# Performance work log

Hardware: AMD Instinct MI355X
Metric: run time of the kernel (lower is better)

The kernel has to match this reference:

```python
import jax, jax.numpy as jnp
import numpy as np

EPS = 1e-12
WA = 0.002


def _radial_bins(h: int, w: int):
    """Static (numpy) replication of torch _radial_masks: centered integer radial
    bins, then fftshift'd (matching the original code exactly)."""
    y = np.linspace(-(h // 2), h // 2 - (1 if h % 2 == 0 else 0), h)
    x = np.linspace(-(w // 2), w // 2 - (1 if w % 2 == 0 else 0), w)
    yy, xx = np.meshgrid(y, x, indexing='ij')
    dist = np.sqrt(xx ** 2 + yy ** 2)
    max_bin = int(dist.max())  # torch: int(max) then clamp -> no-op since dist>=0
    bins = np.clip(dist.astype(np.int32), 0, max_bin)
    bins = np.fft.fftshift(bins)
    return jnp.asarray(bins.reshape(-1)), max_bin


def setup_inputs() -> dict:
    key = jax.random.key(0)
    B, H, W = 16, 1024, 1024
    prob_cg = jax.random.uniform(key, (B, 1, H, W), dtype=jnp.float32)
    return {"prob_cg": prob_cg}


def reference(prob_cg) -> jnp.ndarray:
    B, C, H, W = prob_cg.shape
    seg, max_bin = _radial_bins(H, W)  # [H*W] int32 bin ids, static max_bin
    n_bins = max_bin + 1

    # Power spectrum P(f) = |fftshift(fft2(p))|^2 / N.
    # (torch code fftshifts all dims incl. batch; that is a pure batch permutation
    #  and the final loss is a mean over batch, so shifting only spatial axes is
    #  mathematically identical.)
    p = prob_cg[:, 0].astype(jnp.float32)
    fv = jnp.fft.fftshift(jnp.fft.fft2(p, axes=(-2, -1)), axes=(-2, -1))
    power = (fv.real ** 2 + fv.imag ** 2) / (H * W)  # [B,H,W]

    # Radial segment-mean over integer-radius annuli (replaces the O(B*R*H*W)
    # double loop with a single O(B*H*W) scatter-add).
    flat = power.reshape(B, H * W)
    sums = jax.vmap(lambda v: jax.ops.segment_sum(v, seg, num_segments=n_bins))(flat)
    counts = jax.ops.segment_sum(jnp.ones((H * W,), jnp.float32), seg, num_segments=n_bins)
    radial = jnp.where(counts > 0, sums / jnp.maximum(counts, 1.0), 0.0)  # [B,n_bins]

    # Broadcast radial mean back to the grid and accumulate squared deviation.
    radial_expanded = radial[:, seg].reshape(B, H, W)
    loss = jnp.mean(jnp.sum((power - radial_expanded + EPS) ** 2, axis=(-2, -1)))
    return WA * loss
```

## Files before the change

kernel.cpp:

```cpp
#include <hip/hip_runtime.h>
#include <math.h>

#define NB 16
#define NPAIR 8
#define NBINS 725
#define NPIX (1024*1024)

#define SLOT(idx, c) ((idx)*9 + (c) + ((idx)>>5))
#define SH_SIZE 9248
#define C45 0.70710678118654752f

__device__ __forceinline__ unsigned bf16rn(float f) {
    unsigned u = __float_as_uint(f);
    return (u + 0x7FFFu + ((u >> 16) & 1u)) >> 16;
}
__device__ __forceinline__ unsigned pk2(float2 v) {
    return bf16rn(v.x) | (bf16rn(v.y) << 16);
}
__device__ __forceinline__ float2 up2(unsigned v) {
    return make_float2(__uint_as_float(v << 16), __uint_as_float(v & 0xFFFF0000u));
}

__device__ __forceinline__ constexpr int rev5(int j) {
    return ((j&1)<<4) | ((j&2)<<2) | (j&4) | ((j&8)>>2) | ((j&16)>>4);
}

__device__ __forceinline__ void fft32(float2* r) {
    const float wr[16] = {1.f, 0.98078528f, 0.92387953f, 0.83146961f,
                          0.70710678f, 0.55557023f, 0.38268343f, 0.19509032f,
                          0.f, -0.19509032f, -0.38268343f, -0.55557023f,
                          -0.70710678f, -0.83146961f, -0.92387953f, -0.98078528f};
    const float wi[16] = {0.f, -0.19509032f, -0.38268343f, -0.55557023f,
                          -0.70710678f, -0.83146961f, -0.92387953f, -0.98078528f,
                          -1.f, -0.98078528f, -0.92387953f, -0.83146961f,
                          -0.70710678f, -0.55557023f, -0.38268343f, -0.19509032f};
    #pragma unroll
    for (int s = 1; s <= 5; ++s) {
        const int half = 1 << (s - 1);
        #pragma unroll
        for (int g = 0; g < 32; g += (1 << s)) {
            #pragma unroll
            for (int j = 0; j < half; ++j) {
                const int a = j << (5 - s);
                int i1 = g + j, i2 = i1 + half;
                float2 u = r[i1], v = r[i2], vw;
                if (a == 0)       vw = v;
                else if (a == 8)  vw = make_float2(v.y, -v.x);
                else if (a == 4)  vw = make_float2(C45 * (v.x + v.y), C45 * (v.y - v.x));
                else if (a == 12) vw = make_float2(C45 * (v.y - v.x), -C45 * (v.x + v.y));
                else {
                    const float cw = wr[a], sw = wi[a];
                    vw = make_float2(v.x * cw - v.y * sw, v.x * sw + v.y * cw);
                }
                r[i1] = make_float2(u.x + vw.x, u.y + vw.y);
                r[i2] = make_float2(u.x - vw.x, u.y - vw.y);
            }
        }
    }
}

__device__ __forceinline__ void twiddle1024(float2* r, int n1) {
    float sn, cs;
    sincosf((float)n1 * -0.006135923151542565f, &sn, &cs);
    float wx = 1.f, wy = 0.f;
    #pragma unroll
    for (int k2 = 0; k2 < 32; ++k2) {
        float2 s = r[k2];
        r[k2] = make_float2(s.x * wx - s.y * wy, s.x * wy + s.y * wx);
        float nx = wx * cs - wy * sn;
        wy = wx * sn + wy * cs;
        wx = nx;
    }
}

__device__ __forceinline__ int ibin(int d2) {
    int bin = (int)sqrtf((float)d2);
    if ((bin + 1) * (bin + 1) <= d2) ++bin;
    else if (bin * bin > d2) --bin;
    return bin;
}

__device__ __forceinline__ int col_of(int k, int c) {
    if (k == 0) return (c < 4) ? c : ((c == 4) ? 512 : 1028 - c);
    int a = k << 2;
    return (c < 4) ? (a + c) : (1017 + c - a);
}
__device__ __forceinline__ int mir_of(int k, int c) {
    if (k == 0) return (c == 0 || c == 4) ? c : ((c < 4) ? c + 4 : c - 4);
    return 7 - c;
}

__global__ __launch_bounds__(256, 4) void fft_rows(const float* __restrict__ in,
                                                   unsigned* __restrict__ spec,
                                                   float* __restrict__ cntp) {
    __shared__ unsigned sh[SH_SIZE];
    __shared__ float hc[NBINS];
    int tid = threadIdx.x, blk = blockIdx.x;
    int p = blk >> 7, y0 = (blk & 127) << 3;
    if (p == 0)
        for (int i = tid; i < NBINS; i += 256) hc[i] = 0.f;
    int n1 = tid & 31, c = tid >> 5;
    const float* xr = in + (((size_t)(2 * p)) << 20) + ((size_t)(y0 + c) << 10);
    const float* yr = xr + (1u << 20);
    float2 r[32];
    #pragma unroll
    for (int j = 0; j < 32; ++j) {
        int n = n1 + (rev5(j) << 5);
        r[j] = make_float2(xr[n], yr[n]);
    }
    fft32(r);
    twiddle1024(r, n1);
    int sb = 9 * n1 + c;
    #pragma unroll
    for (int k2 = 0; k2 < 32; ++k2) sh[sb + 289 * k2] = pk2(r[k2]);
    __syncthreads();
    int k2 = tid & 31;
    int rb = 289 * k2 + c;
    #pragma unroll
    for (int j = 0; j < 32; ++j) r[j] = up2(sh[rb + 9 * rev5(j)]);
    fft32(r);
    __syncthreads();
    int wb = 9 * k2 + c;
    #pragma unroll
    for (int k1 = 0; k1 < 32; ++k1) sh[wb + 289 * k1] = pk2(r[k1]);
    __syncthreads();
    unsigned* base = spec + (((size_t)p) << 20);
    for (int rep = 0; rep < 32; ++rep) {
        int idx = (rep << 8) + tid;
        int kcol = idx >> 3, cc = idx & 7;
        base[((size_t)kcol << 10) + y0 + cc] = sh[SLOT(kcol, cc)];
    }
    if (p == 0) {
        int g = blk;
        int row = (g << 2) + (tid >> 6);
        int xb = (tid & 63) << 4;
        int dy = row - 512, dy2 = dy * dy;
        int curbin = -1;
        float a = 0.f;
        #pragma unroll 4
        for (int j = 0; j < 16; ++j) {
            int x = xb + j;
            float w = 2.f;
            if (row == 0) w = (x > 512 || x == 0) ? 0.f : ((x == 512) ? 1.f : 2.f);
            int dx = x - 512;
            int bin = ibin(dy2 + dx * dx);
            if (bin == curbin) a += w;
            else {
                if (curbin >= 0 && a != 0.f) atomicAdd(&hc[curbin], a);
                curbin = bin; a = w;
            }
        }
        if (curbin >= 0 && a != 0.f) atomicAdd(&hc[curbin], a);
        if (g == 0) {
            int xb2 = tid << 2;
            int curb = -1;
            float aa = 0.f;
            #pragma unroll
            for (int j = 0; j < 4; ++j) {
                int xx = xb2 + j;
                if (xx > 512) continue;
                float w = ((xx & 511) == 0) ? 1.f : 2.f;
                int bin = 512 - xx;
                if (bin == curb) aa += w;
                else {
                    if (curb >= 0 && aa != 0.f) atomicAdd(&hc[curb], aa);
                    curb = bin; aa = w;
                }
            }
            if (curb >= 0 && aa != 0.f) atomicAdd(&hc[curb], aa);
        }
        __syncthreads();
        for (int i = tid; i < NBINS; i += 256)
            cntp[(size_t)g * NBINS + i] = hc[i];
    }
}

__global__ __launch_bounds__(256, 3) void fft_cols_hist(const unsigned* __restrict__ spec,
                                                        float* __restrict__ s2buf,
                                                        float* __restrict__ partial) {
    __shared__ unsigned sh[SH_SIZE];
    __shared__ float hs0[NBINS], hs1[NBINS];
    __shared__ float wred[8];
    int tid = threadIdx.x, blk = blockIdx.x;
    int p = blk >> 7, k = blk & 127;
    for (int i = tid; i < NBINS; i += 256) { hs0[i] = 0.f; hs1[i] = 0.f; }
    int n1 = tid & 31, c = tid >> 5;
    const unsigned* base = spec + (((size_t)p) << 20);
    const unsigned* colp = base + ((size_t)col_of(k, c) << 10);
    float2 r[32];
    #pragma unroll
    for (int j = 0; j < 32; ++j) r[j] = up2(colp[n1 + (rev5(j) << 5)]);
    fft32(r);
    twiddle1024(r, n1);
    int sb = 9 * n1 + c;
    #pragma unroll
    for (int q = 0; q < 32; ++q) sh[sb + 289 * q] = pk2(r[q]);
    __syncthreads();
    int k2 = tid & 31;
    int rb = 289 * k2 + c;
    #pragma unroll
    for (int j = 0; j < 32; ++j) r[j] = up2(sh[rb + 9 * rev5(j)]);
    __syncthreads();
    fft32(r);
    int wb = 9 * k2 + c;
    #pragma unroll
    for (int k1 = 0; k1 < 32; ++k1) sh[wb + 289 * k1] = pk2(r[k1]);
    __syncthreads();
    const float inv = 1.0f / (float)NPIX;
    int cl = tid >> 5, chunk = tid & 31;
    int xcol = col_of(k, cl), mc = mir_of(k, cl);
    int dxv = xcol - 512, dx2 = dxv * dxv;
    bool xs = ((xcol & 511) == 0), xhi = (xcol > 512);
    float s2e = 0.f, s2o = 0.f;
    int curbin = -1;
    float a0 = 0.f, a1 = 0.f;
    int ky0 = chunk << 4;
    #pragma unroll 4
    for (int j = 0; j < 16; ++j) {
        int ky = ky0 + j;
        float w = 2.f;
        if (ky == 0) w = xhi ? 0.f : ((xcol == 0) ? 0.f : (xs ? 1.f : 2.f));
        int my = (1024 - ky) & 1023;
        float2 f1 = up2(sh[SLOT(ky, cl)]);
        float2 f2 = up2(sh[SLOT(my, mc)]);
        float xr = 0.5f * (f1.x + f2.x), xi = 0.5f * (f1.y - f2.y);
        float yr = 0.5f * (f1.y + f2.y), yi = 0.5f * (f2.x - f1.x);
        float pe = (xr * xr + xi * xi) * inv;
        float po = (yr * yr + yi * yi) * inv;
        int dy = ky - 512;
        int bin = ibin(dy * dy + dx2);
        float v0 = w * pe, v1 = w * po;
        s2e += v0 * pe;
        s2o += v1 * po;
        if (bin == curbin) { a0 += v0; a1 += v1; }
        else {
            if (curbin >= 0) { atomicAdd(&hs0[curbin], a0); atomicAdd(&hs1[curbin], a1); }
            curbin = bin; a0 = v0; a1 = v1;
        }
    }
    if (curbin >= 0) { atomicAdd(&hs0[curbin], a0); atomicAdd(&hs1[curbin], a1); }
    if ((tid & 31) == 0) {
        int cl2 = tid >> 5;
        int x2 = col_of(k, cl2);
        if (x2 <= 512) {
            int mc2 = mir_of(k, cl2);
            float w = ((x2 & 511) == 0) ? 1.f : 2.f;
            float2 f1 = up2(sh[SLOT(512, cl2)]);
            float2 f2 = up2(sh[SLOT(512, mc2)]);
            float xr = 0.5f * (f1.x + f2.x), xi = 0.5f * (f1.y - f2.y);
            float yr = 0.5f * (f1.y + f2.y), yi = 0.5f * (f2.x - f1.x);
            float pe = (xr * xr + xi * xi) * inv;
            float po = (yr * yr + yi * yi) * inv;
            float v0 = w * pe, v1 = w * po;
            s2e += v0 * pe;
            s2o += v1 * po;
            int bin = (x2 < 512) ? 512 - x2 : 0;
            atomicAdd(&hs0[bin], v0);
            atomicAdd(&hs1[bin], v1);
        }
    }
    #pragma unroll
    for (int off = 32; off > 0; off >>= 1) {
        s2e += __shfl_down(s2e, off);
        s2o += __shfl_down(s2o, off);
    }
    if ((tid & 63) == 0) { wred[tid >> 6] = s2e; wred[4 + (tid >> 6)] = s2o; }
    __syncthreads();
    if (tid == 0) s2buf[2 * blk]     = wred[0] + wred[1] + wred[2] + wred[3];
    if (tid == 1) s2buf[2 * blk + 1] = wred[4] + wred[5] + wred[6] + wred[7];
    float* pe = partial + ((size_t)(2 * p) * 128 + k) * NBINS;
    float* po = partial + ((size_t)(2 * p + 1) * 128 + k) * NBINS;
    for (int i = tid; i < NBINS; i += 256) {
        pe[i] = hs0[i];
        po[i] = hs1[i];
    }
}

__global__ __launch_bounds__(256) void reduce_loss(const float* __restrict__ partial,
                                                   const float* __restrict__ cntp,
                                                   float* __restrict__ rowval) {
    int b = blockIdx.x / 3, band = blockIdx.x % 3;
    int bin = band * 256 + threadIdx.x;
    if (bin >= NBINS) return;
    const float* bp = partial + (size_t)b * 128 * NBINS + bin;
    float s = 0.f;
    #pragma unroll 8
    for (int k = 0; k < 128; ++k) s += bp[(size_t)k * NBINS];
    float cv = 0.f;
    #pragma unroll 8
    for (int g = 0; g < 128; ++g) cv += cntp[(size_t)g * NBINS + bin];
    rowval[b * NBINS + bin] = (cv > 0.f) ? s * s / cv : 0.f;
}

__global__ __launch_bounds__(256) void final_out(const float* __restrict__ s2buf,
                                                 const float* __restrict__ rowval,
                                                 float* __restrict__ out) {
    __shared__ float red[256];
    int tid = threadIdx.x;
    float acc = 0.f;
    for (int i = tid; i < NB * NBINS; i += 256) acc -= rowval[i];
    for (int i = tid; i < 2 * NPAIR * 128; i += 256) acc += s2buf[i];
    red[tid] = acc;
    __syncthreads();
    for (int s = 128; s > 0; s >>= 1) {
        if (tid < s) red[tid] += red[tid + s];
        __syncthreads();
    }
    if (tid == 0) out[0] = red[0] * (0.002f / 16.0f);
}

extern "C" void kernel_launch(void* const* d_in, const int* in_sizes, int n_in,
                              void* d_out, int out_size, void* d_ws, size_t ws_size,
                              hipStream_t stream) {
    const float* in = (const float*)d_in[0];
    float* out = (float*)d_out;
    char* ws = (char*)d_ws;

    unsigned* spec = (unsigned*)ws;
    float* s2buf   = (float*)(ws + ((size_t)NPAIR << 20) * sizeof(unsigned));
    float* rowval  = s2buf + 2 * NPAIR * 128;
    float* cntp    = rowval + NB * NBINS;
    float* partial = cntp + 128 * NBINS;

    fft_rows<<<NPAIR * 128, 256, 0, stream>>>(in, spec, cntp);
    fft_cols_hist<<<NPAIR * 128, 256, 0, stream>>>(spec, s2buf, partial);
    reduce_loss<<<NB * 3, 256, 0, stream>>>(partial, cntp, rowval);
    final_out<<<1, 256, 0, stream>>>(s2buf, rowval, out);
}
```

Baseline: 101.4 us.

## Reuse register FFT outputs for power/histogram and alias histograms into shared buffer

The column-FFT kernel now keeps its own FFT outputs in registers and computes power directly from them. Only the mirrored half-spectrum rows are written to shared memory. The two per-block histograms move out of separate shared arrays into the unused tail of the FFT shared buffer, split into two copies to spread atomic contention. This cuts shared memory so launch bounds can rise to four blocks per CU. In exchange the run-length merging of atomics is dropped, so every element issues its own shared-memory atomic, and a more compact index mapping is assumed.

```diff
diff --git a/kernel.cpp b/kernel.cpp
--- a/kernel.cpp
+++ b/kernel.cpp
@@ -8,6 +8,7 @@
 
 #define SLOT(idx, c) ((idx)*9 + (c) + ((idx)>>5))
 #define SH_SIZE 9248
+#define HSOFF 4672
 #define C45 0.70710678118654752f
 
 __device__ __forceinline__ unsigned bf16rn(float f) {
@@ -175,15 +176,14 @@
     }
 }
 
-__global__ __launch_bounds__(256, 3) void fft_cols_hist(const unsigned* __restrict__ spec,
+__global__ __launch_bounds__(256, 4) void fft_cols_hist(const unsigned* __restrict__ spec,
                                                         float* __restrict__ s2buf,
                                                         float* __restrict__ partial) {
     __shared__ unsigned sh[SH_SIZE];
-    __shared__ float hs0[NBINS], hs1[NBINS];
     __shared__ float wred[8];
+    float* hs = (float*)(sh + HSOFF);
     int tid = threadIdx.x, blk = blockIdx.x;
     int p = blk >> 7, k = blk & 127;
-    for (int i = tid; i < NBINS; i += 256) { hs0[i] = 0.f; hs1[i] = 0.f; }
     int n1 = tid & 31, c = tid >> 5;
     const unsigned* base = spec + (((size_t)p) << 20);
     const unsigned* colp = base + ((size_t)col_of(k, c) << 10);
@@ -202,62 +202,42 @@
     for (int j = 0; j < 32; ++j) r[j] = up2(sh[rb + 9 * rev5(j)]);
     __syncthreads();
     fft32(r);
-    int wb = 9 * k2 + c;
-    #pragma unroll
-    for (int k1 = 0; k1 < 32; ++k1) sh[wb + 289 * k1] = pk2(r[k1]);
+    if (k2 == 0) sh[SLOT(0, c)] = pk2(r[0]);
+    #pragma unroll
+    for (int k1 = 16; k1 < 32; ++k1)
+        sh[SLOT(k2 + (k1 << 5) - 511, c)] = pk2(r[k1]);
+    for (int i = tid; i < 4 * NBINS; i += 256) hs[i] = 0.f;
     __syncthreads();
     const float inv = 1.0f / (float)NPIX;
-    int cl = tid >> 5, chunk = tid & 31;
-    int xcol = col_of(k, cl), mc = mir_of(k, cl);
-    int dxv = xcol - 512, dx2 = dxv * dxv;
-    bool xs = ((xcol & 511) == 0), xhi = (xcol > 512);
+    int x = col_of(k, c), mc = mir_of(k, c);
+    bool xhi = (x > 512), xs = ((x & 511) == 0);
+    int dxv = x - 512, dx2 = dxv * dxv;
+    float* h0 = hs + ((tid >> 6) & 1) * (2 * NBINS);
+    float* h1 = h0 + NBINS;
     float s2e = 0.f, s2o = 0.f;
-    int curbin = -1;
-    float a0 = 0.f, a1 = 0.f;
-    int ky0 = chunk << 4;
-    #pragma unroll 4
-    for (int j = 0; j < 16; ++j) {
-        int ky = ky0 + j;
+    #pragma unroll
+    for (int k1 = 0; k1 < 17; ++k1) {
+        int ky = k2 + (k1 << 5);
+        if (ky > 512) break;
+        bool ek = ((ky & 511) == 0);
         float w = 2.f;
-        if (ky == 0) w = xhi ? 0.f : ((xcol == 0) ? 0.f : (xs ? 1.f : 2.f));
+        if (ek) w = xhi ? 0.f : (xs ? 1.f : 2.f);
+        if (ky == 0 && x == 0) w = 0.f;
         int my = (1024 - ky) & 1023;
-        float2 f1 = up2(sh[SLOT(ky, cl)]);
-        float2 f2 = up2(sh[SLOT(my, mc)]);
-        float xr = 0.5f * (f1.x + f2.x), xi = 0.5f * (f1.y - f2.y);
-        float yr = 0.5f * (f1.y + f2.y), yi = 0.5f * (f2.x - f1.x);
-        float pe = (xr * xr + xi * xi) * inv;
-        float po = (yr * yr + yi * yi) * inv;
-        int dy = ky - 512;
-        int bin = ibin(dy * dy + dx2);
+        int mi = (my == 0) ? 0 : my - 511;
+        float2 f1 = r[k1];
+        float2 f2 = up2(sh[SLOT(mi, mc)]);
+        float xrr = 0.5f * (f1.x + f2.x), xii = 0.5f * (f1.y - f2.y);
+        float yrr = 0.5f * (f1.y + f2.y), yii = 0.5f * (f2.x - f1.x);
+        float pe = (xrr * xrr + xii * xii) * inv;
+        float po = (yrr * yrr + yii * yii) * inv;
         float v0 = w * pe, v1 = w * po;
         s2e += v0 * pe;
         s2o += v1 * po;
-        if (bin == curbin) { a0 += v0; a1 += v1; }
-        else {
-            if (curbin >= 0) { atomicAdd(&hs0[curbin], a0); atomicAdd(&hs1[curbin], a1); }
-            curbin = bin; a0 = v0; a1 = v1;
-        }
-    }
-    if (curbin >= 0) { atomicAdd(&hs0[curbin], a0); atomicAdd(&hs1[curbin], a1); }
-    if ((tid & 31) == 0) {
-        int cl2 = tid >> 5;
-        int x2 = col_of(k, cl2);
-        if (x2 <= 512) {
-            int mc2 = mir_of(k, cl2);
-            float w = ((x2 & 511) == 0) ? 1.f : 2.f;
-            float2 f1 = up2(sh[SLOT(512, cl2)]);
-            float2 f2 = up2(sh[SLOT(512, mc2)]);
-            float xr = 0.5f * (f1.x + f2.x), xi = 0.5f * (f1.y - f2.y);
-            float yr = 0.5f * (f1.y + f2.y), yi = 0.5f * (f2.x - f1.x);
-            float pe = (xr * xr + xi * xi) * inv;
-            float po = (yr * yr + yi * yi) * inv;
-            float v0 = w * pe, v1 = w * po;
-            s2e += v0 * pe;
-            s2o += v1 * po;
-            int bin = (x2 < 512) ? 512 - x2 : 0;
-            atomicAdd(&hs0[bin], v0);
-            atomicAdd(&hs1[bin], v1);
-        }
+        int dy = ky - 512;
+        int bin = ibin(dy * dy + dx2);
+        atomicAdd(&h0[bin], v0);
+        atomicAdd(&h1[bin], v1);
     }
     #pragma unroll
     for (int off = 32; off > 0; off >>= 1) {
@@ -271,8 +251,8 @@
     float* pe = partial + ((size_t)(2 * p) * 128 + k) * NBINS;
     float* po = partial + ((size_t)(2 * p + 1) * 128 + k) * NBINS;
     for (int i = tid; i < NBINS; i += 256) {
-        pe[i] = hs0[i];
-        po[i] = hs1[i];
+        pe[i] = hs[i] + hs[2 * NBINS + i];
+        po[i] = hs[NBINS + i] + hs[3 * NBINS + i];
     }
 }
 
```

New measurement: 116.4 us. 14.8% more time.
